# Kernel tuning notes

Measured on AMD Instinct MI355X. Metric: run time of the kernel, lower is better.

Reference implementation:

```python
import jax, jax.numpy as jnp
import numpy as np

D_MODEL = 256
NUM_HEADS = 8
HEAD_DIM = D_MODEL // NUM_HEADS
WS = 7
BN_EPS = 1e-5


def setup_inputs() -> dict:
    key = jax.random.key(0)
    ks = jax.random.split(key, 5)
    B, C, H, W = 4, D_MODEL, 224, 224
    s = 1.0 / np.sqrt(C)
    return {
        "x": jax.random.normal(ks[0], (B, C, H, W), jnp.float32),
        "Wq": jax.random.normal(ks[1], (C, C), jnp.float32) * s,
        "Wk": jax.random.normal(ks[2], (C, C), jnp.float32) * s,
        "Wv": jax.random.normal(ks[3], (C, C), jnp.float32) * s,
        "Wo": jax.random.normal(ks[4], (C, C), jnp.float32) * s,
        "gamma": jnp.ones((C,), jnp.float32),
        "beta": jnp.zeros((C,), jnp.float32),
    }


def _to_windows(t, B, nh, hd, nHw, nWw):
    # t: (B, C, Hp, Wp) -> (B, nh, nWin, ws*ws, hd)
    t = t.reshape(B, nh, hd, nHw, WS, nWw, WS)
    t = t.transpose(0, 1, 3, 5, 4, 6, 2)  # (B, nh, nHw, nWw, ws, ws, hd)
    return t.reshape(B, nh, nHw * nWw, WS * WS, hd)


def reference(x, Wq, Wk, Wv, Wo, gamma, beta):
    B, C, H, W = x.shape
    pad_h = (-H) % WS
    pad_w = (-W) % WS
    q = jnp.einsum('oc,bchw->bohw', Wq, x)
    k = jnp.einsum('oc,bchw->bohw', Wk, x)
    v = jnpp = jnp.einsum('oc,bchw->bohw', Wv, x)
    if pad_h or pad_w:
        pad = ((0, 0), (0, 0), (0, pad_h), (0, pad_w))
        q, k, v = jnp.pad(q, pad), jnp.pad(k, pad), jnp.pad(v, pad)
    Hp, Wp = H + pad_h, W + pad_w
    nHw, nWw = Hp // WS, Wp // WS
    q_w = _to_windows(q, B, NUM_HEADS, HEAD_DIM, nHw, nWw)
    k_w = _to_windows(k, B, NUM_HEADS, HEAD_DIM, nHw, nWw)
    v_w = _to_windows(v, B, NUM_HEADS, HEAD_DIM, nHw, nWw)
    scale = 1.0 / np.sqrt(HEAD_DIM)
    attn = jnp.einsum('bhnqd,bhnkd->bhnqk', q_w, k_w) * scale
    attn = jax.nn.softmax(attn, axis=-1)
    out_w = jnp.einsum('bhnqk,bhnkd->bhnqd', attn, v_w)
    # fold windows back: (B, nh, nWin, ws*ws, hd) -> (B, C, Hp, Wp)
    out = out_w.reshape(B, NUM_HEADS, nHw, nWw, WS, WS, HEAD_DIM)
    out = out.transpose(0, 1, 6, 2, 4, 3, 5).reshape(B, C, Hp, Wp)
    out = out[:, :, :H, :W]
    out = jnp.einsum('oc,bchw->bohw', Wo, out)
    y = x + out
    # BatchNorm2d (training-mode batch statistics, biased variance)
    mean = jnp.mean(y, axis=(0, 2, 3), keepdims=True)
    var = jnp.mean((y - mean) ** 2, axis=(0, 2, 3), keepdims=True)
    yhat = (y - mean) * jax.lax.rsqrt(var + BN_EPS)
    return yhat * gamma[None, :, None, None] + beta[None, :, None, None]
```

## Files before the change

### kernel.cpp

```cpp
#include <hip/hip_runtime.h>
#include <stdint.h>

typedef __attribute__((ext_vector_type(8))) short short8;
typedef __attribute__((ext_vector_type(4))) float f32x4;

#define MFMA16(a,b,c) __builtin_amdgcn_mfma_f32_16x16x32_bf16((a),(b),(c),0,0,0)

#define GLL16(g, l) __builtin_amdgcn_global_load_lds( \
    (const __attribute__((address_space(1))) void*)(g), \
    (__attribute__((address_space(3))) void*)(l), 16, 0, 0)

__device__ __forceinline__ unsigned short f2bf(float f){
  unsigned u = __builtin_bit_cast(unsigned, f);
  u += 0x7fffu + ((u >> 16) & 1u);
  return (unsigned short)(u >> 16);
}

static constexpr int HW_ = 50176;

__device__ __forceinline__ int panel_off(int r, int c64){
  return r * 64 + ((((c64 >> 3) ^ (r & 7))) << 3) + (c64 & 7);
}

__global__ __launch_bounds__(256) void k_convw(const float* __restrict__ Wq, const float* __restrict__ Wk,
                        const float* __restrict__ Wv, const float* __restrict__ Wo,
                        unsigned short* __restrict__ Wf, unsigned short* __restrict__ Wob){
  int gid = blockIdx.x * 256 + threadIdx.x;
  if (gid < 24576){
    int lane = gid & 63;
    int r1 = gid >> 6;
    int t = r1 % 6;
    int r2 = r1 / 6;
    int kq = r2 & 7, hh = r2 >> 3;
    const float* W = (t < 2) ? Wq : (t < 4) ? Wk : Wv;
    int ch = hh * 32 + (t & 1) * 16 + (lane & 15);
    int k0 = kq * 32 + (lane >> 4) * 8;
    const float* src = W + ch * 256 + k0;
    float4 a = *(const float4*)src, b2 = *(const float4*)(src + 4);
    short8 v;
    v[0]=f2bf(a.x); v[1]=f2bf(a.y); v[2]=f2bf(a.z); v[3]=f2bf(a.w);
    v[4]=f2bf(b2.x); v[5]=f2bf(b2.y); v[6]=f2bf(b2.z); v[7]=f2bf(b2.w);
    *(short8*)(Wf + (size_t)gid * 8) = v;
  } else {
    int og = gid - 24576;
    int o = og >> 5, ck = og & 31;
    const float* src = Wo + o * 256 + ck * 8;
    float4 a = *(const float4*)src, b2 = *(const float4*)(src + 4);
    short8 v;
    v[0]=f2bf(a.x); v[1]=f2bf(a.y); v[2]=f2bf(a.z); v[3]=f2bf(a.w);
    v[4]=f2bf(b2.x); v[5]=f2bf(b2.y); v[6]=f2bf(b2.z); v[7]=f2bf(b2.w);
    int kq = ck >> 3;
    int off = panel_off(o & 127, (ck & 7) * 8);
    *(short8*)(Wob + ((o >> 7) * 4 + kq) * 8192 + off) = v;
  }
}

__global__ __launch_bounds__(512) void k_fused(const float* __restrict__ x,
                                               const unsigned short* __restrict__ Wf,
                                               unsigned short* __restrict__ attnP){
  int bid = blockIdx.x;
  int wg = (bid & 7) * 512 + (bid >> 3);
  int b = wg >> 10;
  int win = wg & 1023;
  int wh = win >> 5, ww = win & 31;
  int tid = threadIdx.x;
  int lane = tid & 63;
  int h = tid >> 6;

  __shared__ __align__(16) unsigned short lds[65536];

  {
    int px = tid & 63, cq = tid >> 6;
    if (px < 49){
      int r = px / 7, cl = px % 7;
      const float* gsrc = x + (size_t)b * 256 * HW_ + (size_t)(wh * 7 + r) * 224 + ww * 7 + cl;
#pragma unroll
      for (int c2 = 0; c2 < 32; ++c2){
        int c = cq * 32 + c2;
        float v = gsrc[(size_t)c * HW_];
        lds[49152 + px * 256 + (((c >> 3) ^ (px & 7)) << 3) + (c & 7)] = f2bf(v);
      }
    } else {
#pragma unroll
      for (int c2 = 0; c2 < 32; ++c2){
        int c = cq * 32 + c2;
        lds[49152 + px * 256 + (((c >> 3) ^ (px & 7)) << 3) + (c & 7)] = 0;
      }
    }
  }
  __syncthreads();

  f32x4 aq[4][2] = {}, ak[4][2] = {}, av[2][4] = {};
  for (int kq = 0; kq < 8; ++kq){
    short8 xf[4];
#pragma unroll
    for (int pt = 0; pt < 4; ++pt){
      int px = pt * 16 + (lane & 15);
      int chk = (kq * 4 + (lane >> 4)) ^ (px & 7);
      xf[pt] = *(const short8*)(lds + 49152 + px * 256 + chk * 8);
    }
    short8 wfr[6];
#pragma unroll
    for (int t = 0; t < 6; ++t)
      wfr[t] = *(const short8*)(Wf + ((size_t)((h * 8 + kq) * 6 + t) * 64 + lane) * 8);
#pragma unroll
    for (int pt = 0; pt < 4; ++pt){
      aq[pt][0] = MFMA16(xf[pt], wfr[0], aq[pt][0]);
      aq[pt][1] = MFMA16(xf[pt], wfr[1], aq[pt][1]);
      ak[pt][0] = MFMA16(xf[pt], wfr[2], ak[pt][0]);
      ak[pt][1] = MFMA16(xf[pt], wfr[3], ak[pt][1]);
      av[0][pt] = MFMA16(wfr[4], xf[pt], av[0][pt]);
      av[1][pt] = MFMA16(wfr[5], xf[pt], av[1][pt]);
    }
  }
#pragma unroll
  for (int pt = 0; pt < 4; ++pt)
#pragma unroll
    for (int t = 0; t < 2; ++t)
#pragma unroll
      for (int j = 0; j < 4; ++j){
        int px = pt * 16 + (lane >> 4) * 4 + j;
        int ch = h * 32 + t * 16 + (lane & 15);
        int pos = px * 256 + (((ch >> 3) ^ (px & 7)) << 3) + (ch & 7);
        lds[pos]         = f2bf(aq[pt][t][j]);
        lds[16384 + pos] = f2bf(ak[pt][t][j]);
      }
#pragma unroll
  for (int ct = 0; ct < 2; ++ct)
#pragma unroll
    for (int pt = 0; pt < 4; ++pt)
#pragma unroll
      for (int j = 0; j < 4; ++j){
        int ch = h * 32 + ct * 16 + (lane >> 4) * 4 + j;
        int px = pt * 16 + (lane & 15);
        lds[32768 + ch * 64 + (((px >> 3) ^ (ch & 7)) << 3) + (px & 7)] = f2bf(av[ct][pt][j]);
      }
  __syncthreads();

  short8 kf[4], qf[4];
#pragma unroll
  for (int i = 0; i < 4; ++i){
    int px = i * 16 + (lane & 15);
    int chk = (h * 4 + (lane >> 4)) ^ (px & 7);
    qf[i] = *(const short8*)(lds + px * 256 + chk * 8);
    kf[i] = *(const short8*)(lds + 16384 + px * 256 + chk * 8);
  }
  f32x4 s[4][4] = {};
#pragma unroll
  for (int mi = 0; mi < 4; ++mi)
#pragma unroll
    for (int ni = 0; ni < 4; ++ni)
      s[mi][ni] = MFMA16(kf[mi], qf[ni], s[mi][ni]);
  __syncthreads();

  const float cexp = 0.25504437f;
  unsigned short* sP = lds + h * 4096;
#pragma unroll
  for (int ni = 0; ni < 4; ++ni){
    float m = -3.0e38f;
#pragma unroll
    for (int mi = 0; mi < 4; ++mi)
#pragma unroll
      for (int r = 0; r < 4; ++r){
        int kp = mi * 16 + ((lane >> 4) * 4) + r;
        if (kp < 49) m = fmaxf(m, s[mi][ni][r]);
      }
    m = fmaxf(m, __shfl_xor(m, 16));
    m = fmaxf(m, __shfl_xor(m, 32));
    float sum = 0.f;
    float pv[4][4];
#pragma unroll
    for (int mi = 0; mi < 4; ++mi)
#pragma unroll
      for (int r = 0; r < 4; ++r){
        int kp = mi * 16 + ((lane >> 4) * 4) + r;
        float e2 = (kp < 49) ? exp2f((s[mi][ni][r] - m) * cexp) : 0.f;
        pv[mi][r] = e2; sum += e2;
      }
    sum += __shfl_xor(sum, 16);
    sum += __shfl_xor(sum, 32);
    float inv = 1.0f / sum;
    int q = ni * 16 + (lane & 15);
#pragma unroll
    for (int mi = 0; mi < 4; ++mi)
#pragma unroll
      for (int r = 0; r < 4; ++r){
        int kp = mi * 16 + ((lane >> 4) * 4) + r;
        int bo = (q * 128 + kp * 2) ^ ((q & 7) << 4);
        sP[bo >> 1] = f2bf(pv[mi][r] * inv);
      }
  }

  f32x4 o[4][2] = {};
#pragma unroll
  for (int kc = 0; kc < 2; ++kc){
    short8 pa[4], vb[2];
#pragma unroll
    for (int mtp = 0; mtp < 4; ++mtp){
      int row = mtp * 16 + (lane & 15);
      int bo = (row * 128 + kc * 64 + (lane >> 4) * 16) ^ ((row & 7) << 4);
      pa[mtp] = *(const short8*)(sP + (bo >> 1));
    }
#pragma unroll
    for (int ntp = 0; ntp < 2; ++ntp){
      int ch = h * 32 + ntp * 16 + (lane & 15);
      int k0 = kc * 32 + (lane >> 4) * 8;
      vb[ntp] = *(const short8*)(lds + 32768 + ch * 64 + (((k0 >> 3) ^ (ch & 7)) << 3));
    }
#pragma unroll
    for (int mtp = 0; mtp < 4; ++mtp)
#pragma unroll
      for (int ntp = 0; ntp < 2; ++ntp)
        o[mtp][ntp] = MFMA16(pa[mtp], vb[ntp], o[mtp][ntp]);
  }
#pragma unroll
  for (int mtp = 0; mtp < 4; ++mtp)
#pragma unroll
    for (int ntp = 0; ntp < 2; ++ntp)
#pragma unroll
      for (int r = 0; r < 4; ++r){
        int px = mtp * 16 + (lane >> 4) * 4 + r;
        int ch = h * 32 + ntp * 16 + (lane & 15);
        lds[49152 + px * 256 + (((ch >> 3) ^ (px & 7)) << 3) + (ch & 7)] = f2bf(o[mtp][ntp][r]);
      }
  __syncthreads();

  size_t pb0 = (size_t)b * 392 * 4;
#pragma unroll
  for (int it = 0; it < 4; ++it){
    int id = it * 512 + tid;
    int px = id >> 5, ck = id & 31;
    if (px < 49){
      short8 v = *(const short8*)(lds + 49152 + px * 256 + ((ck ^ (px & 7)) << 3));
      int pg = (wh * 7 + px / 7) * 224 + ww * 7 + px % 7;
      int nt = pg >> 7, pr = pg & 127;
      size_t off = (pb0 + (size_t)nt * 4 + (ck >> 3)) * 8192 + panel_off(pr, (ck & 7) * 8);
      *(short8*)(attnP + off) = v;
    }
  }
}

__global__ __launch_bounds__(256) void k_gemm_out(const unsigned short* __restrict__ Wp,
                                                  const unsigned short* __restrict__ Bp,
                                                  const float* __restrict__ x,
                                                  float* __restrict__ y,
                                                  float* __restrict__ partials){
  int bid = blockIdx.x;
  int wg = (bid & 7) * 392 + (bid >> 3);
  int mt = wg & 1; int rest = wg >> 1;
  int nt = rest % 392; int b = rest / 392;

  __shared__ __align__(16) unsigned short lds[32768];

  int tid = threadIdx.x;
  int lane = tid & 63;
  int wave = tid >> 6;
  int wm = wave >> 1, wn = wave & 1;

  const unsigned short* Apan = Wp + (size_t)mt * 4 * 8192;
  const unsigned short* Bpan = Bp + ((size_t)(b * 392 + nt)) * 4 * 8192;

  int aoff[2][4], boff[2][4];
#pragma unroll
  for (int kk = 0; kk < 2; ++kk)
#pragma unroll
    for (int i = 0; i < 4; ++i){
      int rowA = wm * 64 + i * 16 + (lane & 15);
      aoff[kk][i] = rowA * 64 + (((kk * 4 + (lane >> 4)) ^ (rowA & 7)) << 3);
      int rowB = wn * 64 + i * 16 + (lane & 15);
      boff[kk][i] = rowB * 64 + (((kk * 4 + (lane >> 4)) ^ (rowB & 7)) << 3);
    }
  int cb = wave * 2048;
  f32x4 acc[4][4] = {};

#pragma unroll
  for (int j = 0; j < 4; ++j){
    int o2 = cb + j * 512;
    GLL16(Apan + o2 + lane * 8, lds + o2);
    GLL16(Bpan + o2 + lane * 8, lds + 8192 + o2);
  }
  __syncthreads();

  int cur = 0;
  for (int kq = 0; kq < 4; ++kq){
    if (kq < 3){
      const unsigned short* Ak = Apan + (kq + 1) * 8192;
      const unsigned short* Bk = Bpan + (kq + 1) * 8192;
      unsigned short* dst = lds + (cur ^ 1) * 16384;
#pragma unroll
      for (int j = 0; j < 4; ++j){
        int o2 = cb + j * 512;
        GLL16(Ak + o2 + lane * 8, dst + o2);
        GLL16(Bk + o2 + lane * 8, dst + 8192 + o2);
      }
    }
    const unsigned short* Alds = lds + cur * 16384;
    const unsigned short* Blds = Alds + 8192;
#pragma unroll
    for (int kk = 0; kk < 2; ++kk){
      short8 af[4], bfv[4];
#pragma unroll
      for (int i = 0; i < 4; ++i) af[i]  = *(const short8*)(Alds + aoff[kk][i]);
#pragma unroll
      for (int j = 0; j < 4; ++j) bfv[j] = *(const short8*)(Blds + boff[kk][j]);
#pragma unroll
      for (int i = 0; i < 4; ++i)
#pragma unroll
        for (int j = 0; j < 4; ++j)
          acc[i][j] = MFMA16(af[i], bfv[j], acc[i][j]);
    }
    __syncthreads();
    cur ^= 1;
  }
  float ps[4][4] = {}, pq[4][4] = {};
#pragma unroll
  for (int i = 0; i < 4; ++i)
#pragma unroll
    for (int j = 0; j < 4; ++j){
      int o = mt * 128 + wm * 64 + i * 16 + (lane >> 4) * 4;
      int p = nt * 128 + wn * 64 + j * 16 + (lane & 15);
      size_t base = ((size_t)(b * 256 + o)) * HW_ + p;
#pragma unroll
      for (int r2 = 0; r2 < 4; ++r2){
        float v = acc[i][j][r2] + x[base + (size_t)r2 * HW_];
        y[base + (size_t)r2 * HW_] = v;
        ps[i][r2] += v;
        pq[i][r2] += v * v;
      }
    }
  float* fl = (float*)lds;
#pragma unroll
  for (int i = 0; i < 4; ++i)
#pragma unroll
    for (int r2 = 0; r2 < 4; ++r2){
      float a = ps[i][r2], q2 = pq[i][r2];
      a += __shfl_xor(a, 1);  q2 += __shfl_xor(q2, 1);
      a += __shfl_xor(a, 2);  q2 += __shfl_xor(q2, 2);
      a += __shfl_xor(a, 4);  q2 += __shfl_xor(q2, 4);
      a += __shfl_xor(a, 8);  q2 += __shfl_xor(q2, 8);
      if ((lane & 15) == 0){
        int cl = wm * 64 + i * 16 + (lane >> 4) * 4 + r2;
        fl[wn * 128 + cl] = a;
        fl[256 + wn * 128 + cl] = q2;
      }
    }
  __syncthreads();
  if (tid < 128){
    partials[(size_t)wg * 256 + tid]       = fl[tid] + fl[128 + tid];
    partials[(size_t)wg * 256 + 128 + tid] = fl[256 + tid] + fl[384 + tid];
  }
}

__global__ __launch_bounds__(256) void k_stats2(const float* __restrict__ partials, float* __restrict__ stats){
  int c = blockIdx.x;
  int mt = c >> 7, cl = c & 127;
  int t = threadIdx.x;
  float s = 0.f, q = 0.f;
  for (int idx = t; idx < 1568; idx += 256){
    const float* p = partials + (size_t)(2 * idx + mt) * 256;
    s += p[cl]; q += p[128 + cl];
  }
  __shared__ float r1[256], r2[256];
  r1[t] = s; r2[t] = q; __syncthreads();
  for (int off = 128; off > 0; off >>= 1){
    if (t < off){ r1[t] += r1[t + off]; r2[t] += r2[t + off]; }
    __syncthreads();
  }
  if (t == 0){
    float mean = r1[0] * (1.f / 200704.f);
    float var  = r2[0] * (1.f / 200704.f) - mean * mean;
    stats[c] = mean;
    stats[256 + c] = rsqrtf(var + 1e-5f);
  }
}

__global__ __launch_bounds__(256) void k_norm(float* __restrict__ y, const float* __restrict__ stats,
                                              const float* __restrict__ gamma, const float* __restrict__ beta){
  const long long total = 12845056LL;
  for (long long idx = (long long)blockIdx.x * 256 + threadIdx.x; idx < total; idx += (long long)gridDim.x * 256){
    int c = (int)((idx / 12544) & 255);
    float sc = stats[256 + c] * gamma[c];
    float sh = beta[c] - stats[c] * sc;
    float4* p = (float4*)y + idx;
    float4 v = *p;
    v.x = v.x * sc + sh; v.y = v.y * sc + sh; v.z = v.z * sc + sh; v.w = v.w * sc + sh;
    *p = v;
  }
}

extern "C" void kernel_launch(void* const* d_in, const int* in_sizes, int n_in,
                              void* d_out, int out_size, void* d_ws, size_t ws_size,
                              hipStream_t stream){
  const float* x     = (const float*)d_in[0];
  const float* Wq    = (const float*)d_in[1];
  const float* Wk    = (const float*)d_in[2];
  const float* Wv    = (const float*)d_in[3];
  const float* Wo    = (const float*)d_in[4];
  const float* gamma = (const float*)d_in[5];
  const float* beta  = (const float*)d_in[6];
  float* out = (float*)d_out;

  char* ws = (char*)d_ws;
  unsigned short* Wf     = (unsigned short*)ws;
  unsigned short* Wo_b   = (unsigned short*)(ws + 393216);
  float*          stats  = (float*)(ws + 524288);
  unsigned short* attnP  = (unsigned short*)(ws + 1048576);
  float*          partials = (float*)(ws + 1048576 + 102760448);

  k_convw<<<128, 256, 0, stream>>>(Wq, Wk, Wv, Wo, Wf, Wo_b);
  k_fused<<<4096, 512, 0, stream>>>(x, Wf, attnP);
  k_gemm_out<<<3136, 256, 0, stream>>>(Wo_b, attnP, x, out, partials);
  k_stats2<<<256, 256, 0, stream>>>(partials, stats);
  k_norm<<<4096, 256, 0, stream>>>(out, stats, gamma, beta);
}
```

Baseline: 495.9 us.

## Pre-transpose input into bf16 windowed layout via separate kernel

Adds a k_xw kernel that reads x with coalesced float4 row loads, converts to bf16, and writes a per-window, channel-swizzled layout. The fused attention kernel then loads each window with global_load_lds 16-byte transfers instead of strided scalar fp32 gathers across 256 channels. This removes the uncoalesced channel-strided reads, but adds an extra kernel launch and a full write plus re-read of a 128MB bf16 intermediate.

```diff
diff --git a/kernel.cpp b/kernel.cpp
--- a/kernel.cpp
+++ b/kernel.cpp
@@ -55,7 +55,48 @@
   }
 }
 
-__global__ __launch_bounds__(512) void k_fused(const float* __restrict__ x,
+__global__ __launch_bounds__(256) void k_xw(const float* __restrict__ x, unsigned short* __restrict__ xw){
+  int bid = blockIdx.x;
+  int cq = bid & 15, wh = (bid >> 4) & 31, b = bid >> 9;
+  __shared__ __align__(16) unsigned short tile[25088];
+  int tid = threadIdx.x;
+  for (int it = 0; it < 25; ++it){
+    int idx = it * 256 + tid;
+    if (idx < 6272){
+      int c = idx & 15;
+      int t2 = idx >> 4;
+      int r = t2 / 56;
+      int w4 = t2 % 56;
+      float4 v = *(const float4*)(x + ((size_t)(b * 256 + cq * 16 + c)) * HW_ + (wh * 7 + r) * 224 + w4 * 4);
+      float vv[4] = {v.x, v.y, v.z, v.w};
+      int w0 = w4 * 4;
+      int ww = w0 / 7;
+      int cl = w0 % 7;
+#pragma unroll
+      for (int i = 0; i < 4; ++i){
+        int px = r * 7 + cl;
+        tile[ww * 784 + px * 16 + (((c >> 3) ^ (px & 1)) << 3) + (c & 7)] = f2bf(vv[i]);
+        if (++cl == 7){ cl = 0; ++ww; }
+      }
+    }
+  }
+  __syncthreads();
+  size_t wb = ((size_t)(b * 1024 + wh * 32)) * 16384;
+  for (int it = 0; it < 13; ++it){
+    int id = it * 256 + tid;
+    if (id < 3136){
+      int ww = id / 98;
+      int rem = id - ww * 98;
+      int px = rem >> 1, half = rem & 1;
+      short8 v = *(const short8*)(tile + ww * 784 + px * 16 + ((half ^ (px & 1)) << 3));
+      int cc = cq * 2 + half;
+      int pos = (cc & 24) | ((cc ^ px) & 7);
+      *(short8*)(xw + wb + (size_t)ww * 16384 + px * 256 + pos * 8) = v;
+    }
+  }
+}
+
+__global__ __launch_bounds__(512) void k_fused(const unsigned short* __restrict__ xw,
                                                const unsigned short* __restrict__ Wf,
                                                unsigned short* __restrict__ attnP){
   int bid = blockIdx.x;
@@ -70,23 +111,20 @@
   __shared__ __align__(16) unsigned short lds[65536];
 
   {
-    int px = tid & 63, cq = tid >> 6;
-    if (px < 49){
-      int r = px / 7, cl = px % 7;
-      const float* gsrc = x + (size_t)b * 256 * HW_ + (size_t)(wh * 7 + r) * 224 + ww * 7 + cl;
-#pragma unroll
-      for (int c2 = 0; c2 < 32; ++c2){
-        int c = cq * 32 + c2;
-        float v = gsrc[(size_t)c * HW_];
-        lds[49152 + px * 256 + (((c >> 3) ^ (px & 7)) << 3) + (c & 7)] = f2bf(v);
-      }
-    } else {
-#pragma unroll
-      for (int c2 = 0; c2 < 32; ++c2){
-        int c = cq * 32 + c2;
-        lds[49152 + px * 256 + (((c >> 3) ^ (px & 7)) << 3) + (c & 7)] = 0;
-      }
-    }
+    if (tid < 448){
+      int rr = 50 + (tid >> 5), ch = tid & 31;
+      short8 z = {};
+      *(short8*)(lds + 49152 + rr * 256 + ch * 8) = z;
+    }
+    const unsigned short* xwin = xw + ((size_t)(b * 1024 + wh * 32 + ww)) * 16384;
+#pragma unroll
+    for (int c3 = 0; c3 < 3; ++c3){
+      int k = c3 * 8 + h;
+      int row = 2 * k + (lane >> 5);
+      GLL16(xwin + row * 256 + (lane & 31) * 8, lds + 49152 + k * 512);
+    }
+    if (h == 0)
+      GLL16(xwin + 48 * 256 + (lane & 31) * 8, lds + 49152 + 24 * 512);
   }
   __syncthreads();
 
@@ -404,11 +442,13 @@
   unsigned short* Wf     = (unsigned short*)ws;
   unsigned short* Wo_b   = (unsigned short*)(ws + 393216);
   float*          stats  = (float*)(ws + 524288);
-  unsigned short* attnP  = (unsigned short*)(ws + 1048576);
-  float*          partials = (float*)(ws + 1048576 + 102760448);
+  unsigned short* xw     = (unsigned short*)(ws + 1048576);
+  unsigned short* attnP  = (unsigned short*)(ws + 1048576 + 134217728);
+  float*          partials = (float*)(ws + 1048576 + 134217728 + 102760448);
 
   k_convw<<<128, 256, 0, stream>>>(Wq, Wk, Wv, Wo, Wf, Wo_b);
-  k_fused<<<4096, 512, 0, stream>>>(x, Wf, attnP);
+  k_xw<<<2048, 256, 0, stream>>>(x, xw);
+  k_fused<<<4096, 512, 0, stream>>>(xw, Wf, attnP);
   k_gemm_out<<<3136, 256, 0, stream>>>(Wo_b, attnP, x, out, partials);
   k_stats2<<<256, 256, 0, stream>>>(partials, stats);
   k_norm<<<4096, 256, 0, stream>>>(out, stats, gamma, beta);
```

After: 521.8 us. 1.05x slower.
